# Kernel optimization log

Hardware: AMD Instinct MI355X
Metric: run time of the kernel (lower is better)

Reference implementation:

```python
import jax, jax.numpy as jnp
import numpy as np

N = 1_000_000
C = 64
H = Wd = 2048
EPS = 1e-5


def _build_neighbors(seed=0):
    """Active-site neighbor map for a 3x3 submanifold conv on an HxW grid.
    Returns int32 [N, 9]; entry = index of active neighbor site, or -1."""
    rng = np.random.default_rng(seed)
    flat = rng.permutation(H * Wd)[:N]            # unique active coords
    grid = np.full(H * Wd, -1, np.int64)
    grid[flat] = np.arange(N)
    ys, xs = flat // Wd, flat % Wd
    cols = []
    for dy in (-1, 0, 1):
        for dx in (-1, 0, 1):
            ny, nx = ys + dy, xs + dx
            valid = (ny >= 0) & (ny < H) & (nx >= 0) & (nx < Wd)
            nf = np.where(valid, np.clip(ny, 0, H - 1) * Wd + np.clip(nx, 0, Wd - 1), 0)
            nb = np.where(valid, grid[nf], -1)    # -1 also if neighbor inactive
            cols.append(nb)
    return np.stack(cols, axis=1).astype(np.int32)


def setup_inputs() -> dict:
    key = jax.random.key(0)
    k1, k2, k3 = jax.random.split(key, 3)
    scale = 1.0 / np.sqrt(9 * C)
    return {
        "features": jax.random.normal(k1, (N, C), jnp.float32),
        "neighbor": jnp.asarray(_build_neighbors()),
        "W1": jax.random.normal(k2, (9, C, C), jnp.float32) * scale,
        "gamma1": jnp.ones((C,), jnp.float32),
        "beta1": jnp.zeros((C,), jnp.float32),
        "W2": jax.random.normal(k3, (9, C, C), jnp.float32) * scale,
        "gamma2": jnp.ones((C,), jnp.float32),
        "beta2": jnp.zeros((C,), jnp.float32),
    }


def _subm_conv(f, W, neighbor):
    # gather -> per-tap GEMM -> accumulate (submanifold: outputs only at active sites)
    out = jnp.zeros_like(f)
    for k in range(9):
        idx = neighbor[:, k]
        mask = (idx >= 0)
        g = jnp.where(mask[:, None], f[jnp.maximum(idx, 0)], 0.0)  # [N, C]
        out = out + g @ W[k]
    return out


def _bn(f, gamma, beta):
    # BatchNorm1d over the active-site axis (training-mode batch statistics)
    m = f.mean(axis=0)
    v = f.var(axis=0)
    return (f - m) * jax.lax.rsqrt(v + EPS) * gamma + beta


def reference(features, neighbor, W1, gamma1, beta1, W2, gamma2, beta2):
    out = _subm_conv(features, W1, neighbor)
    out = jax.nn.relu(_bn(out, gamma1, beta1))
    out = _subm_conv(out, W2, neighbor)
    out = _bn(out, gamma2, beta2) + features
    return jax.nn.relu(out)
```

## Files before the change

kernel.cpp:

```cpp
#include <hip/hip_runtime.h>

#define NSITES 1000000
#define CCH 64
#define EPS_BN 1e-5f

typedef __bf16 bf16x8 __attribute__((ext_vector_type(8)));
typedef float f32x4 __attribute__((ext_vector_type(4)));
typedef unsigned short ushort_t;

__device__ __forceinline__ unsigned short f2bf(float x) {
    __bf16 h = (__bf16)x;
    return __builtin_bit_cast(unsigned short, h);
}
__device__ __forceinline__ float bf2f(unsigned short u) {
    return (float)__builtin_bit_cast(__bf16, u);
}

__global__ void cast_kernel(const float* __restrict__ f, ushort_t* __restrict__ o, int total8) {
    int stride = gridDim.x * blockDim.x;
    for (int i = blockIdx.x * blockDim.x + threadIdx.x; i < total8; i += stride) {
        const float4* fp = (const float4*)(f + (size_t)i * 8);
        float4 v0 = fp[0];
        float4 v1 = fp[1];
        uint4 packed;
        ushort_t* up = (ushort_t*)&packed;
        up[0] = f2bf(v0.x); up[1] = f2bf(v0.y); up[2] = f2bf(v0.z); up[3] = f2bf(v0.w);
        up[4] = f2bf(v1.x); up[5] = f2bf(v1.y); up[6] = f2bf(v1.z); up[7] = f2bf(v1.w);
        *(uint4*)(o + (size_t)i * 8) = packed;
    }
}

__global__ void swizzle_kernel(const float* __restrict__ W1, const float* __restrict__ W2,
                               ushort_t* __restrict__ W1s, ushort_t* __restrict__ W2s) {
    int t = blockIdx.x * blockDim.x + threadIdx.x;
    const float* Wg = W1;
    ushort_t* dst = W1s;
    int u = t;
    if (t >= 36864) { Wg = W2; dst = W2s; u = t - 36864; }
    int j = u & 7;
    int lane = (u >> 3) & 63;
    int nt = (u >> 9) & 3;
    int kk = (u >> 11) & 1;
    int tap = u >> 12;
    int k = 32 * kk + 8 * (lane >> 4) + j;
    int n = 16 * nt + (lane & 15);
    dst[u] = f2bf(Wg[tap * 4096 + k * 64 + n]);
}

__device__ __forceinline__ void gatherA(const ushort_t* __restrict__ fin,
                                        const int (&idxr)[2][9], int t, int quad,
                                        uint4 (&dst)[2][2]) {
#pragma unroll
    for (int mt = 0; mt < 2; ++mt) {
        int id = idxr[mt][t];
        int r = (id < 0) ? NSITES : id;
        const uint4* p = (const uint4*)(fin + ((size_t)r << 6) + (quad << 3));
        dst[mt][0] = p[0];
        dst[mt][1] = p[4];
    }
}

template <bool OUT_BF16>
__global__ __launch_bounds__(256) void conv_kernel(
    const ushort_t* __restrict__ fin,
    const int* __restrict__ nbr,
    const ushort_t* __restrict__ Wsw,
    ushort_t* __restrict__ out_bf, float* __restrict__ out_f,
    float* __restrict__ s_sum, float* __restrict__ s_sq) {

    __shared__ float bs_sum[64];
    __shared__ float bs_sq[64];

    const int tid  = threadIdx.x;
    const int wv   = tid >> 6;
    const int lane = tid & 63;
    const int quad = lane >> 4;
    const int l15  = lane & 15;
    const int sbase = blockIdx.x * 128 + wv * 32;

    if (tid < 64) { bs_sum[tid] = 0.f; bs_sq[tid] = 0.f; }
    __syncthreads();

    int idxr[2][9];
#pragma unroll
    for (int mt = 0; mt < 2; ++mt) {
        int s = sbase + mt * 16 + l15;
        int sc = (s < NSITES) ? s : 0;
        bool sv = (s < NSITES);
#pragma unroll
        for (int t = 0; t < 9; ++t) {
            int id = nbr[(size_t)sc * 9 + t];
            idxr[mt][t] = sv ? id : -1;
        }
    }

    f32x4 acc[2][4];
#pragma unroll
    for (int mt = 0; mt < 2; ++mt)
#pragma unroll
        for (int nt = 0; nt < 4; ++nt) acc[mt][nt] = (f32x4){0.f, 0.f, 0.f, 0.f};

    uint4 abuf[2][2][2];
    gatherA(fin, idxr, 0, quad, abuf[0]);

#pragma unroll
    for (int t = 0; t < 9; ++t) {
        bf16x8 B[2][4];
#pragma unroll
        for (int kk = 0; kk < 2; ++kk)
#pragma unroll
            for (int nt = 0; nt < 4; ++nt)
                B[kk][nt] = *(const bf16x8*)(Wsw + (size_t)(((t * 2 + kk) * 4 + nt) * 64 + lane) * 8);

        if (t < 8) gatherA(fin, idxr, t + 1, quad, abuf[(t + 1) & 1]);

#pragma unroll
        for (int mt = 0; mt < 2; ++mt) {
            bf16x8 a0 = __builtin_bit_cast(bf16x8, abuf[t & 1][mt][0]);
            bf16x8 a1 = __builtin_bit_cast(bf16x8, abuf[t & 1][mt][1]);
#pragma unroll
            for (int nt = 0; nt < 4; ++nt) {
                acc[mt][nt] = __builtin_amdgcn_mfma_f32_16x16x32_bf16(a0, B[0][nt], acc[mt][nt], 0, 0, 0);
                acc[mt][nt] = __builtin_amdgcn_mfma_f32_16x16x32_bf16(a1, B[1][nt], acc[mt][nt], 0, 0, 0);
            }
        }
    }

    float ss[4] = {0.f, 0.f, 0.f, 0.f};
    float sq[4] = {0.f, 0.f, 0.f, 0.f};
#pragma unroll
    for (int mt = 0; mt < 2; ++mt)
#pragma unroll
        for (int nt = 0; nt < 4; ++nt)
#pragma unroll
            for (int r = 0; r < 4; ++r) {
                float v = acc[mt][nt][r];
                ss[nt] += v;
                sq[nt] += v * v;
            }
#pragma unroll
    for (int nt = 0; nt < 4; ++nt) {
        ss[nt] += __shfl_xor(ss[nt], 16);
        ss[nt] += __shfl_xor(ss[nt], 32);
        sq[nt] += __shfl_xor(sq[nt], 16);
        sq[nt] += __shfl_xor(sq[nt], 32);
    }
    if (lane < 16) {
#pragma unroll
        for (int nt = 0; nt < 4; ++nt) {
            atomicAdd(&bs_sum[nt * 16 + l15], ss[nt]);
            atomicAdd(&bs_sq[nt * 16 + l15], sq[nt]);
        }
    }

    if constexpr (OUT_BF16) {
        __shared__ ushort_t tr[4 * 32 * 72];
        ushort_t* w_tr = tr + wv * 32 * 72;
#pragma unroll
        for (int mt = 0; mt < 2; ++mt)
#pragma unroll
            for (int nt = 0; nt < 4; ++nt)
#pragma unroll
                for (int r = 0; r < 4; ++r)
                    w_tr[(mt * 16 + 4 * quad + r) * 72 + nt * 16 + l15] = f2bf(acc[mt][nt][r]);
        int site_s = lane >> 1;
        int half = lane & 1;
        int gs = sbase + site_s;
        if (gs < NSITES) {
#pragma unroll
            for (int c = 0; c < 4; ++c) {
                uint4 d = *(const uint4*)(w_tr + site_s * 72 + half * 32 + c * 8);
                *(uint4*)(out_bf + (size_t)gs * 64 + half * 32 + c * 8) = d;
            }
        }
    } else {
#pragma unroll
        for (int mt = 0; mt < 2; ++mt)
#pragma unroll
            for (int nt = 0; nt < 4; ++nt)
#pragma unroll
                for (int r = 0; r < 4; ++r) {
                    int site = sbase + mt * 16 + 4 * quad + r;
                    if (site < NSITES)
                        out_f[(size_t)site * 64 + nt * 16 + l15] = acc[mt][nt][r];
                }
    }

    __syncthreads();
    if (tid < 64) {
        atomicAdd(&s_sum[tid], bs_sum[tid]);
        atomicAdd(&s_sq[tid], bs_sq[tid]);
    }
}

__global__ void finalize_kernel(const float* __restrict__ sum, const float* __restrict__ sq,
                                const float* __restrict__ gamma, const float* __restrict__ beta,
                                float* __restrict__ a, float* __restrict__ b) {
    int c = threadIdx.x;
    const float invn = 1.0f / (float)NSITES;
    float m = sum[c] * invn;
    float v = sq[c] * invn - m * m;
    float s = gamma[c] * rsqrtf(v + EPS_BN);
    a[c] = s;
    b[c] = beta[c] - m * s;
}

__global__ void act_kernel(ushort_t* __restrict__ h, const float* __restrict__ a,
                           const float* __restrict__ b, int total8) {
    int stride = gridDim.x * blockDim.x;
    for (int i = blockIdx.x * blockDim.x + threadIdx.x; i < total8; i += stride) {
        int c8 = (i & 7) * 8;
        uint4 v = ((const uint4*)h)[i];
        ushort_t* up = (ushort_t*)&v;
#pragma unroll
        for (int j = 0; j < 8; ++j) {
            float x = bf2f(up[j]);
            up[j] = f2bf(fmaxf(a[c8 + j] * x + b[c8 + j], 0.f));
        }
        ((uint4*)h)[i] = v;
    }
}

__global__ void residual_kernel(float* __restrict__ out, const float* __restrict__ feat,
                                const float* __restrict__ a2, const float* __restrict__ b2,
                                int total4) {
    int stride = gridDim.x * blockDim.x;
    for (int i = blockIdx.x * blockDim.x + threadIdx.x; i < total4; i += stride) {
        float4 h = ((const float4*)out)[i];
        float4 f = ((const float4*)feat)[i];
        int c4 = (i & 15) * 4;
        float4 av = *(const float4*)(a2 + c4);
        float4 bv = *(const float4*)(b2 + c4);
        float4 r;
        r.x = fmaxf(av.x * h.x + bv.x + f.x, 0.f);
        r.y = fmaxf(av.y * h.y + bv.y + f.y, 0.f);
        r.z = fmaxf(av.z * h.z + bv.z + f.z, 0.f);
        r.w = fmaxf(av.w * h.w + bv.w + f.w, 0.f);
        ((float4*)out)[i] = r;
    }
}

extern "C" void kernel_launch(void* const* d_in, const int* in_sizes, int n_in,
                              void* d_out, int out_size, void* d_ws, size_t ws_size,
                              hipStream_t stream) {
    const float* features = (const float*)d_in[0];
    const int* nbr        = (const int*)d_in[1];
    const float* W1       = (const float*)d_in[2];
    const float* gamma1   = (const float*)d_in[3];
    const float* beta1    = (const float*)d_in[4];
    const float* W2       = (const float*)d_in[5];
    const float* gamma2   = (const float*)d_in[6];
    const float* beta2    = (const float*)d_in[7];

    char* ws = (char*)d_ws;
    const size_t NB = (size_t)NSITES * CCH * sizeof(unsigned short);

    ushort_t* fbf = (ushort_t*)d_out;
    ushort_t* h1  = (ushort_t*)ws;
    size_t off = NB + 512;
    ushort_t* W1s = (ushort_t*)(ws + off);
    ushort_t* W2s = (ushort_t*)(ws + off + 147456);
    float* stats  = (float*)(ws + off + 294912);
    float* ab     = (float*)(ws + off + 294912 + 1024);

    hipMemsetAsync(stats, 0, 256 * sizeof(float), stream);
    hipMemsetAsync(fbf + (size_t)NSITES * 64, 0, 128, stream);
    hipMemsetAsync(h1 + (size_t)NSITES * 64, 0, 128, stream);

    cast_kernel<<<8192, 256, 0, stream>>>(features, fbf, NSITES * CCH / 8);
    swizzle_kernel<<<288, 256, 0, stream>>>(W1, W2, W1s, W2s);

    const int nblk = (NSITES + 127) / 128;
    conv_kernel<true><<<nblk, 256, 0, stream>>>(
        fbf, nbr, W1s, h1, nullptr, stats + 0, stats + 64);
    finalize_kernel<<<1, 64, 0, stream>>>(stats + 0, stats + 64, gamma1, beta1, ab + 0, ab + 64);

    act_kernel<<<8192, 256, 0, stream>>>(h1, ab + 0, ab + 64, NSITES * CCH / 8);

    conv_kernel<false><<<nblk, 256, 0, stream>>>(
        h1, nbr, W2s, nullptr, (float*)d_out, stats + 128, stats + 192);
    finalize_kernel<<<1, 64, 0, stream>>>(stats + 128, stats + 192, gamma2, beta2, ab + 128, ab + 192);

    residual_kernel<<<8192, 256, 0, stream>>>((float*)d_out, features, ab + 128, ab + 192,
                                              NSITES * CCH / 4);
}
```

Before: 1.088 ms.

## Deepen gather prefetch to three stages and widen elementwise kernel vectors

The conv kernel now prefetches neighbor feature rows two taps ahead using a triple buffer. It splits the weight loads per K-half so the next tap's first half loads during the current MFMAs, and wraps the MFMA block in s_setprio. The cast, activation and residual kernels each handle twice as many elements per thread with wider vector loads and stores. The aim is to hide gather latency in the memory-bound conv and cut loop overhead in the elementwise passes, at the cost of more live registers in the conv kernel, which may lower occupancy.

```diff
diff --git a/kernel.cpp b/kernel.cpp
--- a/kernel.cpp
+++ b/kernel.cpp
@@ -16,17 +16,24 @@
     return (float)__builtin_bit_cast(__bf16, u);
 }
 
-__global__ void cast_kernel(const float* __restrict__ f, ushort_t* __restrict__ o, int total8) {
+__global__ void cast_kernel(const float* __restrict__ f, ushort_t* __restrict__ o, int total16) {
     int stride = gridDim.x * blockDim.x;
-    for (int i = blockIdx.x * blockDim.x + threadIdx.x; i < total8; i += stride) {
-        const float4* fp = (const float4*)(f + (size_t)i * 8);
+    for (int i = blockIdx.x * blockDim.x + threadIdx.x; i < total16; i += stride) {
+        const float4* fp = (const float4*)(f + (size_t)i * 16);
         float4 v0 = fp[0];
         float4 v1 = fp[1];
-        uint4 packed;
-        ushort_t* up = (ushort_t*)&packed;
+        float4 v2 = fp[2];
+        float4 v3 = fp[3];
+        uint4 pa, pb;
+        ushort_t* up = (ushort_t*)&pa;
         up[0] = f2bf(v0.x); up[1] = f2bf(v0.y); up[2] = f2bf(v0.z); up[3] = f2bf(v0.w);
         up[4] = f2bf(v1.x); up[5] = f2bf(v1.y); up[6] = f2bf(v1.z); up[7] = f2bf(v1.w);
-        *(uint4*)(o + (size_t)i * 8) = packed;
+        ushort_t* uq = (ushort_t*)&pb;
+        uq[0] = f2bf(v2.x); uq[1] = f2bf(v2.y); uq[2] = f2bf(v2.z); uq[3] = f2bf(v2.w);
+        uq[4] = f2bf(v3.x); uq[5] = f2bf(v3.y); uq[6] = f2bf(v3.z); uq[7] = f2bf(v3.w);
+        uint4* op = (uint4*)(o + (size_t)i * 16);
+        op[0] = pa;
+        op[1] = pb;
     }
 }
 
@@ -60,6 +67,13 @@
     }
 }
 
+__device__ __forceinline__ void loadB(const ushort_t* __restrict__ Wsw, int t, int kk, int lane,
+                                      bf16x8 (&B)[4]) {
+#pragma unroll
+    for (int nt = 0; nt < 4; ++nt)
+        B[nt] = *(const bf16x8*)(Wsw + (size_t)(((t * 2 + kk) * 4 + nt) * 64 + lane) * 8);
+}
+
 template <bool OUT_BF16>
 __global__ __launch_bounds__(256) void conv_kernel(
     const ushort_t* __restrict__ fin,
@@ -100,29 +114,43 @@
 #pragma unroll
         for (int nt = 0; nt < 4; ++nt) acc[mt][nt] = (f32x4){0.f, 0.f, 0.f, 0.f};
 
-    uint4 abuf[2][2][2];
+    uint4 abuf[3][2][2];
     gatherA(fin, idxr, 0, quad, abuf[0]);
+    gatherA(fin, idxr, 1, quad, abuf[1]);
+
+    bf16x8 B0[4];
+    loadB(Wsw, 0, 0, lane, B0);
 
 #pragma unroll
     for (int t = 0; t < 9; ++t) {
-        bf16x8 B[2][4];
-#pragma unroll
-        for (int kk = 0; kk < 2; ++kk)
+        bf16x8 B1[4];
+        loadB(Wsw, t, 1, lane, B1);
+
+        if (t < 7) gatherA(fin, idxr, t + 2, quad, abuf[(t + 2) % 3]);
+
+        bf16x8 B0n[4];
+        if (t < 8) loadB(Wsw, t + 1, 0, lane, B0n);
+
+        __builtin_amdgcn_s_setprio(1);
+#pragma unroll
+        for (int mt = 0; mt < 2; ++mt) {
+            bf16x8 a0 = __builtin_bit_cast(bf16x8, abuf[t % 3][mt][0]);
 #pragma unroll
             for (int nt = 0; nt < 4; ++nt)
-                B[kk][nt] = *(const bf16x8*)(Wsw + (size_t)(((t * 2 + kk) * 4 + nt) * 64 + lane) * 8);
-
-        if (t < 8) gatherA(fin, idxr, t + 1, quad, abuf[(t + 1) & 1]);
-
+                acc[mt][nt] = __builtin_amdgcn_mfma_f32_16x16x32_bf16(a0, B0[nt], acc[mt][nt], 0, 0, 0);
+        }
 #pragma unroll
         for (int mt = 0; mt < 2; ++mt) {
-            bf16x8 a0 = __builtin_bit_cast(bf16x8, abuf[t & 1][mt][0]);
-            bf16x8 a1 = __builtin_bit_cast(bf16x8, abuf[t & 1][mt][1]);
-#pragma unroll
-            for (int nt = 0; nt < 4; ++nt) {
-                acc[mt][nt] = __builtin_amdgcn_mfma_f32_16x16x32_bf16(a0, B[0][nt], acc[mt][nt], 0, 0, 0);
-                acc[mt][nt] = __builtin_amdgcn_mfma_f32_16x16x32_bf16(a1, B[1][nt], acc[mt][nt], 0, 0, 0);
-            }
+            bf16x8 a1 = __builtin_bit_cast(bf16x8, abuf[t % 3][mt][1]);
+#pragma unroll
+            for (int nt = 0; nt < 4; ++nt)
+                acc[mt][nt] = __builtin_amdgcn_mfma_f32_16x16x32_bf16(a1, B1[nt], acc[mt][nt], 0, 0, 0);
+        }
+        __builtin_amdgcn_s_setprio(0);
+
+        if (t < 8) {
+#pragma unroll
+            for (int nt = 0; nt < 4; ++nt) B0[nt] = B0n[nt];
         }
     }
 
@@ -206,37 +234,63 @@
 }
 
 __global__ void act_kernel(ushort_t* __restrict__ h, const float* __restrict__ a,
-                           const float* __restrict__ b, int total8) {
+                           const float* __restrict__ b, int total16) {
+    int stride = gridDim.x * blockDim.x;
+    for (int i = blockIdx.x * blockDim.x + threadIdx.x; i < total16; i += stride) {
+        int c16 = (i & 3) * 16;
+        uint4* hp = (uint4*)(h + (size_t)i * 16);
+        uint4 v0 = hp[0];
+        uint4 v1 = hp[1];
+        float av[16], bv[16];
+#pragma unroll
+        for (int q = 0; q < 4; ++q) {
+            *(float4*)&av[q * 4] = *(const float4*)(a + c16 + q * 4);
+            *(float4*)&bv[q * 4] = *(const float4*)(b + c16 + q * 4);
+        }
+        ushort_t* up = (ushort_t*)&v0;
+#pragma unroll
+        for (int j = 0; j < 8; ++j) {
+            float x = bf2f(up[j]);
+            up[j] = f2bf(fmaxf(av[j] * x + bv[j], 0.f));
+        }
+        ushort_t* uq = (ushort_t*)&v1;
+#pragma unroll
+        for (int j = 0; j < 8; ++j) {
+            float x = bf2f(uq[j]);
+            uq[j] = f2bf(fmaxf(av[8 + j] * x + bv[8 + j], 0.f));
+        }
+        hp[0] = v0;
+        hp[1] = v1;
+    }
+}
+
+__global__ void residual_kernel(float* __restrict__ out, const float* __restrict__ feat,
+                                const float* __restrict__ a2, const float* __restrict__ b2,
+                                int total8) {
     int stride = gridDim.x * blockDim.x;
     for (int i = blockIdx.x * blockDim.x + threadIdx.x; i < total8; i += stride) {
+        float4* op = (float4*)(out + (size_t)i * 8);
+        const float4* fp = (const float4*)(feat + (size_t)i * 8);
+        float4 h0 = op[0];
+        float4 h1v = op[1];
+        float4 f0 = fp[0];
+        float4 f1 = fp[1];
         int c8 = (i & 7) * 8;
-        uint4 v = ((const uint4*)h)[i];
-        ushort_t* up = (ushort_t*)&v;
-#pragma unroll
-        for (int j = 0; j < 8; ++j) {
-            float x = bf2f(up[j]);
-            up[j] = f2bf(fmaxf(a[c8 + j] * x + b[c8 + j], 0.f));
-        }
-        ((uint4*)h)[i] = v;
-    }
-}
-
-__global__ void residual_kernel(float* __restrict__ out, const float* __restrict__ feat,
-                                const float* __restrict__ a2, const float* __restrict__ b2,
-                                int total4) {
-    int stride = gridDim.x * blockDim.x;
-    for (int i = blockIdx.x * blockDim.x + threadIdx.x; i < total4; i += stride) {
-        float4 h = ((const float4*)out)[i];
-        float4 f = ((const float4*)feat)[i];
-        int c4 = (i & 15) * 4;
-        float4 av = *(const float4*)(a2 + c4);
-        float4 bv = *(const float4*)(b2 + c4);
-        float4 r;
-        r.x = fmaxf(av.x * h.x + bv.x + f.x, 0.f);
-        r.y = fmaxf(av.y * h.y + bv.y + f.y, 0.f);
-        r.z = fmaxf(av.z * h.z + bv.z + f.z, 0.f);
-        r.w = fmaxf(av.w * h.w + bv.w + f.w, 0.f);
-        ((float4*)out)[i] = r;
+        float4 av0 = *(const float4*)(a2 + c8);
+        float4 av1 = *(const float4*)(a2 + c8 + 4);
+        float4 bv0 = *(const float4*)(b2 + c8);
+        float4 bv1 = *(const float4*)(b2 + c8 + 4);
+        float4 r0, r1;
+        r0.x = fmaxf(av0.x * h0.x + bv0.x + f0.x, 0.f);
+        r0.y = fmaxf(av0.y * h0.y + bv0.y + f0.y, 0.f);
+        r0.z = fmaxf(av0.z * h0.z + bv0.z + f0.z, 0.f);
+        r0.w = fmaxf(av0.w * h0.w + bv0.w + f0.w, 0.f);
+        r1.x = fmaxf(av1.x * h1v.x + bv1.x + f1.x, 0.f);
+        r1.y = fmaxf(av1.y * h1v.y + bv1.y + f1.y, 0.f);
+        r1.z = fmaxf(av1.z * h1v.z + bv1.z + f1.z, 0.f);
+        r1.w = fmaxf(av1.w * h1v.w + bv1.w + f1.w, 0.f);
+        op[0] = r0;
+        op[1] = r1;
     }
 }
 
@@ -267,7 +321,7 @@
     hipMemsetAsync(fbf + (size_t)NSITES * 64, 0, 128, stream);
     hipMemsetAsync(h1 + (size_t)NSITES * 64, 0, 128, stream);
 
-    cast_kernel<<<8192, 256, 0, stream>>>(features, fbf, NSITES * CCH / 8);
+    cast_kernel<<<8192, 256, 0, stream>>>(features, fbf, NSITES * CCH / 16);
     swizzle_kernel<<<288, 256, 0, stream>>>(W1, W2, W1s, W2s);
 
     const int nblk = (NSITES + 127) / 128;
@@ -275,12 +329,12 @@
         fbf, nbr, W1s, h1, nullptr, stats + 0, stats + 64);
     finalize_kernel<<<1, 64, 0, stream>>>(stats + 0, stats + 64, gamma1, beta1, ab + 0, ab + 64);
 
-    act_kernel<<<8192, 256, 0, stream>>>(h1, ab + 0, ab + 64, NSITES * CCH / 8);
+    act_kernel<<<8192, 256, 0, stream>>>(h1, ab + 0, ab + 64, NSITES * CCH / 16);
 
     conv_kernel<false><<<nblk, 256, 0, stream>>>(
         h1, nbr, W2s, nullptr, (float*)d_out, stats + 128, stats + 192);
     finalize_kernel<<<1, 64, 0, stream>>>(stats + 128, stats + 192, gamma2, beta2, ab + 128, ab + 192);
 
     residual_kernel<<<8192, 256, 0, stream>>>((float*)d_out, features, ab + 128, ab + 192,
-                                              NSITES * CCH / 4);
-}
+                                              NSITES * CCH / 8);
+}
```

After: 1.099 ms. About the same (+1.0%).
